# Kernel optimization log

Measured on AMD Instinct MI355X. Metric: run time of the kernel, lower is better.

Reference implementation:

```python
import jax, jax.numpy as jnp
import numpy as np

V, D, H, L, FF, T, B, W = 32000, 1024, 16, 8, 4096, 1024, 2, 256
HALF = FF // 2
HD = D // H
EPS = 1e-5


def layer_norm(x, g, b):
    mu = jnp.mean(x, axis=-1, keepdims=True)
    var = jnp.mean(jnp.square(x - mu), axis=-1, keepdims=True)
    return (x - mu) * jax.lax.rsqrt(var + EPS) * g + b


def setup_inputs() -> dict:
    key = jax.random.key(0)
    ks = jax.random.split(key, 12)
    s = 0.02
    nrm = lambda k, shape: jax.random.normal(k, shape, jnp.float32) * s
    idx = jax.random.randint(ks[0], (B, T), 0, V, dtype=jnp.int64)
    return {
        "idx": idx,
        "tok_emb": nrm(ks[1], (V, D)),
        "pos_emb": nrm(ks[2], (T, D)),
        "ln1_g": jnp.ones((L, D), jnp.float32),
        "ln1_b": jnp.zeros((L, D), jnp.float32),
        "qkv_w": nrm(ks[3], (L, 3 * D, D)),
        "out_w": nrm(ks[4], (L, D, D)),
        "ln2_g": jnp.ones((L, D), jnp.float32),
        "ln2_b": jnp.zeros((L, D), jnp.float32),
        "a_w1": nrm(ks[5], (L, HALF, D)),
        "a_w2": nrm(ks[6], (L, D, HALF)),
        "f_w1": nrm(ks[7], (L, HALF, D)),
        "f_w2": nrm(ks[8], (L, D, HALF)),
        "lnf_g": jnp.ones((D,), jnp.float32),
        "lnf_b": jnp.zeros((D,), jnp.float32),
        "head_w": nrm(ks[9], (V, D)),
    }


def _forward(idx, tok_emb, pos_emb, ln1_g, ln1_b, qkv_w, out_w, ln2_g, ln2_b,
             a_w1, a_w2, f_w1, f_w2, lnf_g, lnf_b, head_w):
    Bc, Tc = idx.shape
    x = tok_emb[idx] + pos_emb[:Tc]  # [B,T,D]
    # sliding-window causal band: attend to j in [i-W+1, i]
    i = jnp.arange(Tc)
    d = i[:, None] - i[None, :]
    mask = jnp.where((d >= 0) & (d < W), 0.0, -jnp.inf).astype(x.dtype)  # [T,T]
    scale = 1.0 / np.sqrt(HD)

    def block(x, p):
        l1g, l1b, qw, ow, l2g, l2b, aw1, aw2, fw1, fw2 = p
        h = layer_norm(x, l1g, l1b)
        qkv = (h @ qw.T).reshape(Bc, Tc, 3, H, HD)
        q, k, v = qkv[:, :, 0], qkv[:, :, 1], qkv[:, :, 2]  # [B,T,H,HD]
        attn = jnp.einsum('bqhd,bkhd->bhqk', q, k) * scale + mask
        attn = jax.nn.softmax(attn, axis=-1)
        o = jnp.einsum('bhqk,bkhd->bqhd', attn, v).reshape(Bc, Tc, D)
        x = x + o @ ow.T
        h2 = layer_norm(x, l2g, l2b)
        mlp = (jax.nn.gelu(h2 @ aw1.T, approximate=False) @ aw2.T
               + jax.nn.gelu(h2 @ fw1.T, approximate=False) @ fw2.T)
        return x + mlp, None

    x, _ = jax.lax.scan(block, x, (ln1_g, ln1_b, qkv_w, out_w, ln2_g, ln2_b,
                                   a_w1, a_w2, f_w1, f_w2))
    return layer_norm(x, lnf_g, lnf_b) @ head_w.T  # [B,T,V]


def reference(idx, tok_emb, pos_emb, ln1_g, ln1_b, qkv_w, out_w, ln2_g, ln2_b,
              a_w1, a_w2, f_w1, f_w2, lnf_g, lnf_b, head_w):
    return _forward(idx, tok_emb, pos_emb, ln1_g, ln1_b, qkv_w, out_w,
                    ln2_g, ln2_b, a_w1, a_w2, f_w1, f_w2, lnf_g, lnf_b, head_w)
```

## Files before the change

kernel.cpp:

```cpp
#include <hip/hip_runtime.h>

typedef __bf16 bf16x8 __attribute__((ext_vector_type(8)));
typedef __bf16 bf16x4 __attribute__((ext_vector_type(4)));
typedef float  f32x4  __attribute__((ext_vector_type(4)));
typedef unsigned int u32x4 __attribute__((ext_vector_type(4)));

#define MFMA16(a, b, c) __builtin_amdgcn_mfma_f32_16x16x32_bf16(a, b, c, 0, 0, 0)

__device__ __forceinline__ void gload_lds16(const void* g, void* l) {
  __builtin_amdgcn_global_load_lds(
      (const __attribute__((address_space(1))) void*)g,
      (__attribute__((address_space(3))) void*)l, 16, 0, 0);
}

__global__ __launch_bounds__(256) void cvt_kernel(
    const float* __restrict__ s, __bf16* __restrict__ d, int n8) {
  int i = blockIdx.x * 256 + threadIdx.x;
  if (i >= n8) return;
  size_t o = (size_t)i * 8;
  f32x4 a = *(const f32x4*)(s + o), b = *(const f32x4*)(s + o + 4);
  bf16x8 v;
  v[0] = (__bf16)a[0]; v[1] = (__bf16)a[1]; v[2] = (__bf16)a[2]; v[3] = (__bf16)a[3];
  v[4] = (__bf16)b[0]; v[5] = (__bf16)b[1]; v[6] = (__bf16)b[2]; v[7] = (__bf16)b[3];
  *(bf16x8*)(d + o) = v;
}

__global__ __launch_bounds__(256) void cat_w1_kernel(
    const float* __restrict__ a, const float* __restrict__ f, __bf16* __restrict__ d) {
  int i = blockIdx.x * 256 + threadIdx.x;
  int k = (i & 127) * 8;
  int r = i >> 7;
  const float* s = (r < 2048) ? a + ((size_t)r << 10) + k
                              : f + ((size_t)(r - 2048) << 10) + k;
  f32x4 va = *(const f32x4*)s, vb = *(const f32x4*)(s + 4);
  bf16x8 v;
  v[0] = (__bf16)va[0]; v[1] = (__bf16)va[1]; v[2] = (__bf16)va[2]; v[3] = (__bf16)va[3];
  v[4] = (__bf16)vb[0]; v[5] = (__bf16)vb[1]; v[6] = (__bf16)vb[2]; v[7] = (__bf16)vb[3];
  *(bf16x8*)(d + ((size_t)i << 3)) = v;
}

__global__ __launch_bounds__(256) void cat_w2_kernel(
    const float* __restrict__ a, const float* __restrict__ f, __bf16* __restrict__ d) {
  int i = blockIdx.x * 256 + threadIdx.x;
  int k = (i & 511) * 8;
  int r = i >> 9;
  const float* s = (k < 2048) ? a + (size_t)r * 2048 + k
                              : f + (size_t)r * 2048 + (k - 2048);
  f32x4 va = *(const f32x4*)s, vb = *(const f32x4*)(s + 4);
  bf16x8 v;
  v[0] = (__bf16)va[0]; v[1] = (__bf16)va[1]; v[2] = (__bf16)va[2]; v[3] = (__bf16)va[3];
  v[4] = (__bf16)vb[0]; v[5] = (__bf16)vb[1]; v[6] = (__bf16)vb[2]; v[7] = (__bf16)vb[3];
  *(bf16x8*)(d + ((size_t)i << 3)) = v;
}

__global__ __launch_bounds__(256) void embed_kernel(
    const int* __restrict__ idx, const float* __restrict__ te,
    const float* __restrict__ pe, float* __restrict__ x) {
  int m = blockIdx.x;
  int t = m & 1023;
  int tok = idx[m];
  int c = threadIdx.x * 4;
  f32x4 a = *(const f32x4*)(te + (size_t)tok * 1024 + c);
  f32x4 p = *(const f32x4*)(pe + (size_t)t * 1024 + c);
  *(f32x4*)(x + (size_t)m * 1024 + c) = a + p;
}

__global__ __launch_bounds__(256) void ln_kernel(
    const float* __restrict__ x, const float* __restrict__ g,
    const float* __restrict__ bb, __bf16* __restrict__ out) {
  int row = blockIdx.x, tid = threadIdx.x;
  int wid = tid >> 6, lane = tid & 63;
  f32x4 v = *(const f32x4*)(x + (size_t)row * 1024 + tid * 4);
  float s = v[0] + v[1] + v[2] + v[3];
  #pragma unroll
  for (int off = 32; off >= 1; off >>= 1) s += __shfl_xor(s, off);
  __shared__ float red1[4], red2[4];
  if (lane == 0) red1[wid] = s;
  __syncthreads();
  float mu = (red1[0] + red1[1] + red1[2] + red1[3]) * (1.0f / 1024.0f);
  float d0 = v[0] - mu, d1 = v[1] - mu, d2 = v[2] - mu, d3 = v[3] - mu;
  float q = d0 * d0 + d1 * d1 + d2 * d2 + d3 * d3;
  #pragma unroll
  for (int off = 32; off >= 1; off >>= 1) q += __shfl_xor(q, off);
  if (lane == 0) red2[wid] = q;
  __syncthreads();
  float var = (red2[0] + red2[1] + red2[2] + red2[3]) * (1.0f / 1024.0f);
  float inv = rsqrtf(var + 1e-5f);
  f32x4 gg = *(const f32x4*)(g + tid * 4);
  f32x4 bv = *(const f32x4*)(bb + tid * 4);
  bf16x4 o4;
  o4[0] = (__bf16)(d0 * inv * gg[0] + bv[0]);
  o4[1] = (__bf16)(d1 * inv * gg[1] + bv[1]);
  o4[2] = (__bf16)(d2 * inv * gg[2] + bv[2]);
  o4[3] = (__bf16)(d3 * inv * gg[3] + bv[3]);
  *(bf16x4*)(out + (size_t)row * 1024 + tid * 4) = o4;
}

template <int BN, int EPI>
__global__ __launch_bounds__(256) void gemm_bf16(
    const __bf16* __restrict__ A, int lda,
    const __bf16* __restrict__ B, int ldb, int K,
    float* __restrict__ Cf, __bf16* __restrict__ Cb, int ldc,
    const float* __restrict__ resid, int nbx) {
  constexpr int ACCN = BN / 32;
  __shared__ __align__(16) __bf16 As[128 * 32];
  __shared__ __align__(16) __bf16 Bs[BN * 32];

  int nwg = gridDim.x;
  int id = blockIdx.x;
  int q = nwg >> 3, r = nwg & 7;
  int xcd = id & 7, pos = id >> 3;
  int nid = (xcd < r ? xcd * (q + 1) : r * (q + 1) + (xcd - r) * q) + pos;
  int row0 = (nid % nbx) * 128;
  int col0 = (nid / nbx) * BN;

  const int tid = threadIdx.x, lane = tid & 63, wid = tid >> 6;
  const int l15 = lane & 15, l4 = lane >> 4;
  const int wr = wid >> 1, wc = wid & 1;

  f32x4 acc[4][ACCN];
  #pragma unroll
  for (int i = 0; i < 4; ++i)
    #pragma unroll
    for (int j = 0; j < ACCN; ++j) acc[i][j] = (f32x4){0.f, 0.f, 0.f, 0.f};

  const __bf16* aptr = A + (size_t)row0 * lda;
  const __bf16* bptr = B + (size_t)col0 * ldb;

  for (int k0 = 0; k0 < K; k0 += 32) {
    #pragma unroll
    for (int i = 0; i < 2; ++i) {
      int ch = tid + 256 * i;
      gload_lds16(aptr + (size_t)(ch >> 2) * lda + k0 + (ch & 3) * 8, &As[ch * 8]);
    }
    #pragma unroll
    for (int i = 0; i < BN / 64; ++i) {
      int ch = tid + 256 * i;
      gload_lds16(bptr + (size_t)(ch >> 2) * ldb + k0 + (ch & 3) * 8, &Bs[ch * 8]);
    }
    __syncthreads();
    bf16x8 af[4], bfr[ACCN];
    #pragma unroll
    for (int mi = 0; mi < 4; ++mi)
      af[mi] = *(const bf16x8*)&As[(wr * 64 + mi * 16 + l15) * 32 + l4 * 8];
    #pragma unroll
    for (int ni = 0; ni < ACCN; ++ni)
      bfr[ni] = *(const bf16x8*)&Bs[(wc * (BN / 2) + ni * 16 + l15) * 32 + l4 * 8];
    #pragma unroll
    for (int mi = 0; mi < 4; ++mi)
      #pragma unroll
      for (int ni = 0; ni < ACCN; ++ni)
        acc[mi][ni] = MFMA16(af[mi], bfr[ni], acc[mi][ni]);
    __syncthreads();
  }

  #pragma unroll
  for (int mi = 0; mi < 4; ++mi)
    #pragma unroll
    for (int ni = 0; ni < ACCN; ++ni)
      #pragma unroll
      for (int rr = 0; rr < 4; ++rr) {
        int row = row0 + wr * 64 + mi * 16 + l4 * 4 + rr;
        int col = col0 + wc * (BN / 2) + ni * 16 + l15;
        float v = acc[mi][ni][rr];
        size_t off = (size_t)row * ldc + col;
        if (EPI == 0) {
          Cf[off] = v;
        } else if (EPI == 1) {
          Cb[off] = (__bf16)v;
        } else if (EPI == 2) {
          float gv = 0.5f * v * (1.0f + erff(v * 0.70710678118654752f));
          Cb[off] = (__bf16)gv;
        } else {
          Cf[off] = resid[off] + v;
        }
      }
}

__global__ __launch_bounds__(256) void attn_kernel(
    const __bf16* __restrict__ qkv, __bf16* __restrict__ o) {
  const int bid = blockIdx.x;
  const int qt = bid & 15, h = (bid >> 4) & 15, b = bid >> 8;
  const int qs = qt * 64;
  const int ntiles = (qt + 1 < 5) ? (qt + 1) : 5;
  const int kt0 = qt - (ntiles - 1);

  __shared__ __align__(16) __bf16 Qs[64][72];
  __shared__ __align__(16) __bf16 KVs[64][72];
  __shared__ __align__(16) __bf16 Ssm[64][328];
  __shared__ float rsum[64];

  const int tid = threadIdx.x;
  const int lane = tid & 63, wid = tid >> 6;
  const int l15 = lane & 15, l4 = lane >> 4;
  const size_t rs = 3072;
  const __bf16* qbase = qkv + ((size_t)(b * 1024 + qs)) * rs + h * 64;

  #pragma unroll
  for (int i = 0; i < 2; ++i) {
    int c = tid * 2 + i;
    int rr = c >> 3, dc = c & 7;
    *(u32x4*)&Qs[rr][dc * 8] = *(const u32x4*)(qbase + (size_t)rr * rs + dc * 8);
  }

  for (int it = 0; it < ntiles; ++it) {
    int kt = kt0 + it;
    const __bf16* kbase = qkv + ((size_t)(b * 1024 + kt * 64)) * rs + 1024 + h * 64;
    __syncthreads();
    #pragma unroll
    for (int i = 0; i < 2; ++i) {
      int c = tid * 2 + i;
      int rr = c >> 3, dc = c & 7;
      *(u32x4*)&KVs[rr][dc * 8] = *(const u32x4*)(kbase + (size_t)rr * rs + dc * 8);
    }
    __syncthreads();
    bf16x8 aq[2];
    #pragma unroll
    for (int kk = 0; kk < 2; ++kk)
      aq[kk] = *(const bf16x8*)&Qs[16 * wid + l15][kk * 32 + l4 * 8];
    #pragma unroll
    for (int n = 0; n < 4; ++n) {
      f32x4 c4 = (f32x4){0.f, 0.f, 0.f, 0.f};
      #pragma unroll
      for (int kk = 0; kk < 2; ++kk) {
        bf16x8 bk = *(const bf16x8*)&KVs[n * 16 + l15][kk * 32 + l4 * 8];
        c4 = MFMA16(aq[kk], bk, c4);
      }
      int kj = kt * 64 + n * 16 + l15;
      int colS = it * 64 + n * 16 + l15;
      #pragma unroll
      for (int rr = 0; rr < 4; ++rr) {
        int qi = qs + 16 * wid + l4 * 4 + rr;
        int d = qi - kj;
        float sv = c4[rr] * 0.125f;
        Ssm[16 * wid + l4 * 4 + rr][colS] =
            (d >= 0 && d < 256) ? (__bf16)sv : (__bf16)(-1e30f);
      }
    }
  }

  for (int rr = 0; rr < 16; ++rr) {
    int row = 16 * wid + rr;
    float vals[5];
    #pragma unroll
    for (int i = 0; i < 5; ++i) vals[i] = -3e38f;
    #pragma unroll
    for (int i = 0; i < 5; ++i)
      if (i < ntiles) vals[i] = (float)Ssm[row][lane + 64 * i];
    float m = vals[0];
    #pragma unroll
    for (int i = 1; i < 5; ++i) m = fmaxf(m, vals[i]);
    #pragma unroll
    for (int off = 32; off >= 1; off >>= 1) m = fmaxf(m, __shfl_xor(m, off));
    float s = 0.f;
    #pragma unroll
    for (int i = 0; i < 5; ++i)
      if (i < ntiles) {
        float p = __expf(vals[i] - m);
        s += p;
        Ssm[row][lane + 64 * i] = (__bf16)p;
      }
    #pragma unroll
    for (int off = 32; off >= 1; off >>= 1) s += __shfl_xor(s, off);
    if (lane == 0) rsum[row] = s;
  }

  f32x4 oacc[4];
  #pragma unroll
  for (int n = 0; n < 4; ++n) oacc[n] = (f32x4){0.f, 0.f, 0.f, 0.f};

  for (int it = 0; it < ntiles; ++it) {
    int kt = kt0 + it;
    const __bf16* vbase = qkv + ((size_t)(b * 1024 + kt * 64)) * rs + 2048 + h * 64;
    __syncthreads();
    if (tid < 64) {
      int k0 = (tid >> 3) * 8, d0 = (tid & 7) * 8;
      bf16x8 vr[8];
      #pragma unroll
      for (int rr = 0; rr < 8; ++rr)
        vr[rr] = *(const bf16x8*)(vbase + (size_t)(k0 + rr) * rs + d0);
      #pragma unroll
      for (int j = 0; j < 8; ++j) {
        bf16x8 w;
        #pragma unroll
        for (int rr = 0; rr < 8; ++rr) w[rr] = vr[rr][j];
        *(bf16x8*)&KVs[d0 + j][k0] = w;
      }
    }
    __syncthreads();
    #pragma unroll
    for (int kk = 0; kk < 2; ++kk) {
      bf16x8 ap = *(const bf16x8*)&Ssm[16 * wid + l15][it * 64 + kk * 32 + l4 * 8];
      #pragma unroll
      for (int n = 0; n < 4; ++n) {
        bf16x8 bv = *(const bf16x8*)&KVs[n * 16 + l15][kk * 32 + l4 * 8];
        oacc[n] = MFMA16(ap, bv, oacc[n]);
      }
    }
  }

  #pragma unroll
  for (int n = 0; n < 4; ++n)
    #pragma unroll
    for (int rr = 0; rr < 4; ++rr) {
      int qrow = 16 * wid + l4 * 4 + rr;
      float inv = 1.0f / rsum[qrow];
      size_t m = (size_t)(b * 1024 + qs + qrow);
      o[m * 1024 + h * 64 + n * 16 + l15] = (__bf16)(oacc[n][rr] * inv);
    }
}

extern "C" void kernel_launch(void* const* d_in, const int* in_sizes, int n_in,
                              void* d_out, int out_size, void* d_ws, size_t ws_size,
                              hipStream_t stream) {
  (void)in_sizes; (void)n_in; (void)out_size;
  const int*   idx     = (const int*)d_in[0];
  const float* tok_emb = (const float*)d_in[1];
  const float* pos_emb = (const float*)d_in[2];
  const float* ln1_g   = (const float*)d_in[3];
  const float* ln1_b   = (const float*)d_in[4];
  const float* qkv_w   = (const float*)d_in[5];
  const float* out_w   = (const float*)d_in[6];
  const float* ln2_g   = (const float*)d_in[7];
  const float* ln2_b   = (const float*)d_in[8];
  const float* a_w1    = (const float*)d_in[9];
  const float* a_w2    = (const float*)d_in[10];
  const float* f_w1    = (const float*)d_in[11];
  const float* f_w2    = (const float*)d_in[12];
  const float* lnf_g   = (const float*)d_in[13];
  const float* lnf_b   = (const float*)d_in[14];
  const float* head_w  = (const float*)d_in[15];
  float* out = (float*)d_out;

  char* ws = (char*)d_ws;
  float*  x    = (float*)(ws);
  __bf16* h    = (__bf16*)(ws + 8388608);
  __bf16* qkv  = (__bf16*)(ws + 12582912);
  __bf16* oatt = (__bf16*)(ws + 25165824);
  __bf16* gcat = (__bf16*)(ws + 29360128);

  const bool full = ws_size >= 313000000ull;

  __bf16 *wq, *wo, *w1c, *w2c, *wh;
  if (full) {
    wq  = (__bf16*)(ws + 46137344);
    wo  = (__bf16*)(ws + 96468992);
    w1c = (__bf16*)(ws + 113246208);
    w2c = (__bf16*)(ws + 180355072);
    wh  = (__bf16*)(ws + 247463936);
    cvt_kernel<<<12288, 256, 0, stream>>>(qkv_w, wq, 3145728);
    cvt_kernel<<<4096, 256, 0, stream>>>(out_w, wo, 1048576);
    for (int l = 0; l < 8; ++l) {
      cat_w1_kernel<<<2048, 256, 0, stream>>>(
          a_w1 + (size_t)l * 2048 * 1024, f_w1 + (size_t)l * 2048 * 1024,
          w1c + (size_t)l * 4096 * 1024);
      cat_w2_kernel<<<2048, 256, 0, stream>>>(
          a_w2 + (size_t)l * 1024 * 2048, f_w2 + (size_t)l * 1024 * 2048,
          w2c + (size_t)l * 1024 * 4096);
    }
    cvt_kernel<<<16000, 256, 0, stream>>>(head_w, wh, 4096000);
  } else {
    wq  = (__bf16*)(ws + 46137344);
    wo  = (__bf16*)(ws + 52428800);
    w1c = (__bf16*)(ws + 54525952);
    w2c = (__bf16*)(ws + 62914560);
    wh  = (__bf16*)(ws + 46137344);
  }

  embed_kernel<<<2048, 256, 0, stream>>>(idx, tok_emb, pos_emb, x);

  for (int l = 0; l < 8; ++l) {
    const __bf16 *wq_l, *wo_l, *w1_l, *w2_l;
    if (full) {
      wq_l = wq + (size_t)l * 3072 * 1024;
      wo_l = wo + (size_t)l * 1024 * 1024;
      w1_l = w1c + (size_t)l * 4096 * 1024;
      w2_l = w2c + (size_t)l * 1024 * 4096;
    } else {
      cvt_kernel<<<1536, 256, 0, stream>>>(qkv_w + (size_t)l * 3072 * 1024, wq, 393216);
      cvt_kernel<<<512, 256, 0, stream>>>(out_w + (size_t)l * 1024 * 1024, wo, 131072);
      cat_w1_kernel<<<2048, 256, 0, stream>>>(
          a_w1 + (size_t)l * 2048 * 1024, f_w1 + (size_t)l * 2048 * 1024, w1c);
      cat_w2_kernel<<<2048, 256, 0, stream>>>(
          a_w2 + (size_t)l * 1024 * 2048, f_w2 + (size_t)l * 1024 * 2048, w2c);
      wq_l = wq; wo_l = wo; w1_l = w1c; w2_l = w2c;
    }

    ln_kernel<<<2048, 256, 0, stream>>>(x, ln1_g + l * 1024, ln1_b + l * 1024, h);
    gemm_bf16<128, 1><<<16 * 24, 256, 0, stream>>>(
        h, 1024, wq_l, 1024, 1024, nullptr, qkv, 3072, nullptr, 16);
    attn_kernel<<<512, 256, 0, stream>>>(qkv, oatt);
    gemm_bf16<64, 3><<<16 * 16, 256, 0, stream>>>(
        oatt, 1024, wo_l, 1024, 1024, x, nullptr, 1024, x, 16);
    ln_kernel<<<2048, 256, 0, stream>>>(x, ln2_g + l * 1024, ln2_b + l * 1024, h);
    gemm_bf16<128, 2><<<16 * 32, 256, 0, stream>>>(
        h, 1024, w1_l, 1024, 1024, nullptr, gcat, 4096, nullptr, 16);
    gemm_bf16<64, 3><<<16 * 16, 256, 0, stream>>>(
        gcat, 4096, w2_l, 4096, 4096, x, nullptr, 1024, x, 16);
  }

  if (!full) {
    cvt_kernel<<<16000, 256, 0, stream>>>(head_w, wh, 4096000);
  }
  ln_kernel<<<2048, 256, 0, stream>>>(x, lnf_g, lnf_b, h);
  gemm_bf16<128, 0><<<16 * 250, 256, 0, stream>>>(
      h, 1024, wh, 1024, 1024, out, nullptr, 32000, nullptr, 16);
}
```

Measured before the change: 2.230 ms.

## Add 256x256 triple-buffered GEMM and double-buffer existing GEMM with swizzled LDS

Measured after the change: 2.082 ms. 6.6% less time.

```diff
diff --git a/kernel.cpp b/kernel.cpp
--- a/kernel.cpp
+++ b/kernel.cpp
@@ -11,6 +11,13 @@
   __builtin_amdgcn_global_load_lds(
       (const __attribute__((address_space(1))) void*)g,
       (__attribute__((address_space(3))) void*)l, 16, 0, 0);
+}
+
+__device__ __forceinline__ void waitvm(int vm) {
+  if (vm == 6)      asm volatile("s_waitcnt vmcnt(6)" ::: "memory");
+  else if (vm == 4) asm volatile("s_waitcnt vmcnt(4)" ::: "memory");
+  else if (vm == 3) asm volatile("s_waitcnt vmcnt(3)" ::: "memory");
+  else              asm volatile("s_waitcnt vmcnt(0)" ::: "memory");
 }
 
 __global__ __launch_bounds__(256) void cvt_kernel(
@@ -96,6 +103,126 @@
   *(bf16x4*)(out + (size_t)row * 1024 + tid * 4) = o4;
 }
 
+template <int EPI>
+__global__ __launch_bounds__(512, 2) void gemm256(
+    const __bf16* __restrict__ A, int lda,
+    const __bf16* __restrict__ B, int ldb, int K,
+    float* __restrict__ Cf, __bf16* __restrict__ Cb, int ldc, int nbx) {
+  __shared__ __align__(16) __bf16 lds[49152];
+  const int tid = threadIdx.x, lane = tid & 63, w = tid >> 6;
+  const int l15 = lane & 15, l4 = lane >> 4;
+  const int wr = w >> 2, wc = w & 3;
+
+  int nwg = gridDim.x, id = blockIdx.x;
+  int q = nwg >> 3, r = nwg & 7;
+  int xcd = id & 7, pos = id >> 3;
+  int nid = (xcd < r ? xcd * (q + 1) : r * (q + 1) + (xcd - r) * q) + pos;
+  int row0 = (nid % nbx) * 256, col0 = (nid / nbx) * 256;
+
+  const __bf16* ag = A + (size_t)row0 * lda;
+  const __bf16* bg = B + (size_t)col0 * ldb;
+
+  f32x4 acc[8][4];
+  #pragma unroll
+  for (int i = 0; i < 8; ++i)
+    #pragma unroll
+    for (int j = 0; j < 4; ++j) acc[i][j] = (f32x4){0.f, 0.f, 0.f, 0.f};
+
+  int srow[2], scol[2];
+  #pragma unroll
+  for (int i = 0; i < 2; ++i) {
+    int p = (w + i * 8) * 1024 + lane * 16;
+    int row = p >> 6, ch = (p >> 4) & 3;
+    srow[i] = row;
+    scol[i] = (ch ^ ((row >> 1) & 3)) * 8;
+  }
+  const int fx = (((l4 << 4) ^ (((l15 >> 1) & 3) << 4)) >> 1);
+
+  auto stageA = [&](int t, int c) {
+    #pragma unroll
+    for (int i = 0; i < 2; ++i)
+      gload_lds16(ag + (size_t)srow[i] * lda + t * 32 + scol[i],
+                  &lds[c * 16384 + (w + i * 8) * 512]);
+  };
+  auto stageB = [&](int t, int c) {
+    #pragma unroll
+    for (int i = 0; i < 2; ++i)
+      gload_lds16(bg + (size_t)srow[i] * ldb + t * 32 + scol[i],
+                  &lds[c * 16384 + 8192 + (w + i * 8) * 512]);
+  };
+
+  auto kgroup = [&](int t2, int c, int cn, int vm, bool stg) {
+    if (stg) stageA(t2, cn);
+    waitvm(vm);
+    __builtin_amdgcn_sched_barrier(0);
+    __builtin_amdgcn_s_barrier();
+    __builtin_amdgcn_sched_barrier(0);
+    const int cb = c * 16384;
+    bf16x8 bfr[4], af[4];
+    #pragma unroll
+    for (int ni = 0; ni < 4; ++ni)
+      bfr[ni] = *(const bf16x8*)&lds[cb + 8192 + (wc * 64 + ni * 16 + l15) * 32 + fx];
+    #pragma unroll
+    for (int mi = 0; mi < 4; ++mi)
+      af[mi] = *(const bf16x8*)&lds[cb + (wr * 128 + mi * 16 + l15) * 32 + fx];
+    __builtin_amdgcn_s_setprio(1);
+    #pragma unroll
+    for (int mi = 0; mi < 4; ++mi)
+      #pragma unroll
+      for (int ni = 0; ni < 4; ++ni)
+        acc[mi][ni] = MFMA16(af[mi], bfr[ni], acc[mi][ni]);
+    __builtin_amdgcn_s_setprio(0);
+    #pragma unroll
+    for (int mi = 0; mi < 4; ++mi)
+      af[mi] = *(const bf16x8*)&lds[cb + (wr * 128 + (mi + 4) * 16 + l15) * 32 + fx];
+    if (stg) stageB(t2, cn);
+    __builtin_amdgcn_s_setprio(1);
+    #pragma unroll
+    for (int mi = 0; mi < 4; ++mi)
+      #pragma unroll
+      for (int ni = 0; ni < 4; ++ni)
+        acc[mi + 4][ni] = MFMA16(af[mi], bfr[ni], acc[mi + 4][ni]);
+    __builtin_amdgcn_s_setprio(0);
+    __builtin_amdgcn_sched_barrier(0);
+    __builtin_amdgcn_s_barrier();
+    __builtin_amdgcn_sched_barrier(0);
+  };
+
+  const int NT = K >> 5;
+  stageA(0, 0); stageB(0, 0);
+  stageA(1, 1); stageB(1, 1);
+
+  int c = 0;
+  for (int t = 0; t < NT - 2; ++t) {
+    int cn = c + 2; if (cn >= 3) cn -= 3;
+    kgroup(t + 2, c, cn, 6, true);
+    c = (c == 2) ? 0 : c + 1;
+  }
+  kgroup(0, c, 0, 4, false);
+  c = (c == 2) ? 0 : c + 1;
+  kgroup(0, c, 0, 0, false);
+
+  #pragma unroll
+  for (int mi = 0; mi < 8; ++mi)
+    #pragma unroll
+    for (int ni = 0; ni < 4; ++ni)
+      #pragma unroll
+      for (int rr = 0; rr < 4; ++rr) {
+        int row = row0 + wr * 128 + mi * 16 + l4 * 4 + rr;
+        int col = col0 + wc * 64 + ni * 16 + l15;
+        float v = acc[mi][ni][rr];
+        size_t off = (size_t)row * ldc + col;
+        if (EPI == 0) {
+          Cf[off] = v;
+        } else if (EPI == 1) {
+          Cb[off] = (__bf16)v;
+        } else {
+          float gv = 0.5f * v * (1.0f + erff(v * 0.70710678118654752f));
+          Cb[off] = (__bf16)gv;
+        }
+      }
+}
+
 template <int BN, int EPI>
 __global__ __launch_bounds__(256) void gemm_bf16(
     const __bf16* __restrict__ A, int lda,
@@ -103,11 +230,12 @@
     float* __restrict__ Cf, __bf16* __restrict__ Cb, int ldc,
     const float* __restrict__ resid, int nbx) {
   constexpr int ACCN = BN / 32;
-  __shared__ __align__(16) __bf16 As[128 * 32];
-  __shared__ __align__(16) __bf16 Bs[BN * 32];
-
-  int nwg = gridDim.x;
-  int id = blockIdx.x;
+  constexpr int LB = BN / 64;
+  constexpr int L = 2 + LB;
+  __shared__ __align__(16) __bf16 As[2 * 4096];
+  __shared__ __align__(16) __bf16 Bs[2 * BN * 32];
+
+  int nwg = gridDim.x, id = blockIdx.x;
   int q = nwg >> 3, r = nwg & 7;
   int xcd = id & 7, pos = id >> 3;
   int nid = (xcd < r ? xcd * (q + 1) : r * (q + 1) + (xcd - r) * q) + pos;
@@ -117,6 +245,7 @@
   const int tid = threadIdx.x, lane = tid & 63, wid = tid >> 6;
   const int l15 = lane & 15, l4 = lane >> 4;
   const int wr = wid >> 1, wc = wid & 1;
+  const int fx = (((l4 << 4) ^ (((l15 >> 1) & 3) << 4)) >> 1);
 
   f32x4 acc[4][ACCN];
   #pragma unroll
@@ -127,31 +256,48 @@
   const __bf16* aptr = A + (size_t)row0 * lda;
   const __bf16* bptr = B + (size_t)col0 * ldb;
 
-  for (int k0 = 0; k0 < K; k0 += 32) {
+  auto stage = [&](int t, int p) {
     #pragma unroll
     for (int i = 0; i < 2; ++i) {
       int ch = tid + 256 * i;
-      gload_lds16(aptr + (size_t)(ch >> 2) * lda + k0 + (ch & 3) * 8, &As[ch * 8]);
-    }
-    #pragma unroll
-    for (int i = 0; i < BN / 64; ++i) {
+      int rr = ch >> 2, kc = ch & 3;
+      gload_lds16(aptr + (size_t)rr * lda + t * 32 + (kc ^ ((rr >> 1) & 3)) * 8,
+                  &As[p * 4096 + ch * 8]);
+    }
+    #pragma unroll
+    for (int i = 0; i < LB; ++i) {
       int ch = tid + 256 * i;
-      gload_lds16(bptr + (size_t)(ch >> 2) * ldb + k0 + (ch & 3) * 8, &Bs[ch * 8]);
-    }
-    __syncthreads();
+      int rr = ch >> 2, kc = ch & 3;
+      gload_lds16(bptr + (size_t)rr * ldb + t * 32 + (kc ^ ((rr >> 1) & 3)) * 8,
+                  &Bs[p * BN * 32 + ch * 8]);
+    }
+  };
+
+  const int NT = K >> 5;
+  stage(0, 0);
+  for (int t = 0; t < NT; ++t) {
+    int p = t & 1;
+    bool stg = (t + 1 < NT);
+    if (stg) stage(t + 1, p ^ 1);
+    waitvm(stg ? L : 0);
+    __builtin_amdgcn_sched_barrier(0);
+    __builtin_amdgcn_s_barrier();
+    __builtin_amdgcn_sched_barrier(0);
     bf16x8 af[4], bfr[ACCN];
     #pragma unroll
     for (int mi = 0; mi < 4; ++mi)
-      af[mi] = *(const bf16x8*)&As[(wr * 64 + mi * 16 + l15) * 32 + l4 * 8];
+      af[mi] = *(const bf16x8*)&As[p * 4096 + (wr * 64 + mi * 16 + l15) * 32 + fx];
     #pragma unroll
     for (int ni = 0; ni < ACCN; ++ni)
-      bfr[ni] = *(const bf16x8*)&Bs[(wc * (BN / 2) + ni * 16 + l15) * 32 + l4 * 8];
+      bfr[ni] = *(const bf16x8*)&Bs[p * BN * 32 + (wc * (BN / 2) + ni * 16 + l15) * 32 + fx];
     #pragma unroll
     for (int mi = 0; mi < 4; ++mi)
       #pragma unroll
       for (int ni = 0; ni < ACCN; ++ni)
         acc[mi][ni] = MFMA16(af[mi], bfr[ni], acc[mi][ni]);
-    __syncthreads();
+    __builtin_amdgcn_sched_barrier(0);
+    __builtin_amdgcn_s_barrier();
+    __builtin_amdgcn_sched_barrier(0);
   }
 
   #pragma unroll
@@ -387,14 +533,14 @@
     }
 
     ln_kernel<<<2048, 256, 0, stream>>>(x, ln1_g + l * 1024, ln1_b + l * 1024, h);
-    gemm_bf16<128, 1><<<16 * 24, 256, 0, stream>>>(
-        h, 1024, wq_l, 1024, 1024, nullptr, qkv, 3072, nullptr, 16);
+    gemm256<1><<<8 * 12, 512, 0, stream>>>(
+        h, 1024, wq_l, 1024, 1024, nullptr, qkv, 3072, 8);
     attn_kernel<<<512, 256, 0, stream>>>(qkv, oatt);
     gemm_bf16<64, 3><<<16 * 16, 256, 0, stream>>>(
         oatt, 1024, wo_l, 1024, 1024, x, nullptr, 1024, x, 16);
     ln_kernel<<<2048, 256, 0, stream>>>(x, ln2_g + l * 1024, ln2_b + l * 1024, h);
-    gemm_bf16<128, 2><<<16 * 32, 256, 0, stream>>>(
-        h, 1024, w1_l, 1024, 1024, nullptr, gcat, 4096, nullptr, 16);
+    gemm256<2><<<8 * 16, 512, 0, stream>>>(
+        h, 1024, w1_l, 1024, 1024, nullptr, gcat, 4096, 8);
     gemm_bf16<64, 3><<<16 * 16, 256, 0, stream>>>(
         gcat, 4096, w2_l, 4096, 4096, x, nullptr, 1024, x, 16);
   }
@@ -403,6 +549,6 @@
     cvt_kernel<<<16000, 256, 0, stream>>>(head_w, wh, 4096000);
   }
   ln_kernel<<<2048, 256, 0, stream>>>(x, lnf_g, lnf_b, h);
-  gemm_bf16<128, 0><<<16 * 250, 256, 0, stream>>>(
-      h, 1024, wh, 1024, 1024, out, nullptr, 32000, nullptr, 16);
-}
+  gemm256<0><<<8 * 125, 512, 0, stream>>>(
+      h, 1024, wh, 1024, 1024, out, nullptr, 32000, 8);
+}
```
